# Kernel tuning notes

Measured on AMD Instinct MI355X. Metric: run time of the kernel, lower is better.

Reference implementation:

```python
import jax, jax.numpy as jnp
import numpy as np

BAND_LOW_MAX = 500.0
BAND_MID_MAX = 2000.0
ENERGY_THRESHOLD = 0.5

V, NH, NM = 1024, 16384, 16384


def setup_inputs() -> dict:
    key = jax.random.key(0)
    k1, k2, k3, k4, k5, k6 = jax.random.split(key, 6)
    harm_amps = jax.random.uniform(k1, (V, NH), dtype=jnp.float32)
    noise_mags = jax.random.uniform(k2, (V, NM), dtype=jnp.float32)
    # fundamental in [50, 1000) Hz so low/mid/high bands are all populated
    f0_hz = 50.0 + 950.0 * jax.random.uniform(k3, (V,), dtype=jnp.float32)
    competition_weight = 0.1 + jax.random.uniform(k4, (V,), dtype=jnp.float32)
    withdrawal = jax.random.uniform(k5, (V, 3), dtype=jnp.float32)  # [low, mid, high]
    is_active = jax.random.randint(k6, (V,), 0, 2).astype(bool)
    return {
        'harm_amps': harm_amps,
        'noise_mags': noise_mags,
        'f0_hz': f0_hz,
        'competition_weight': competition_weight,
        'withdrawal': withdrawal,
        'is_active': is_active,
    }


def reference(harm_amps, noise_mags, f0_hz, competition_weight, withdrawal, is_active):
    dt = harm_amps.dtype
    nh = harm_amps.shape[-1]
    actf = is_active.astype(dt)                     # [V]
    n_active = jnp.sum(is_active)

    harmonics = jnp.arange(1, nh + 1, dtype=dt)     # [NH]
    freqs = f0_hz[:, None] * harmonics[None, :]     # [V, NH]
    # bands partition the harmonics: 0=low (<500), 1=mid [500,2000), 2=high (>=2000)
    band_idx = (freqs >= BAND_LOW_MAX).astype(jnp.int32) + (freqs >= BAND_MID_MAX).astype(jnp.int32)  # [V, NH]

    # per-voice per-band energy (inactive voices contribute 0, as in the torch code)
    energy = jnp.stack(
        [jnp.sum(jnp.where(band_idx == b, harm_amps, jnp.zeros((), dt)), axis=-1) for b in range(3)],
        axis=1,
    ) * actf[:, None]                               # [V, 3]

    total_energy = jnp.sum(energy, axis=0)          # [3]
    total_weight = jnp.sum(competition_weight * actf)

    claim_ratio = competition_weight / jnp.maximum(total_weight, 1e-6)  # [V]
    my_share = claim_ratio * ENERGY_THRESHOLD                           # [V]
    excess = energy - my_share[:, None]                                 # [V, 3]
    excess_ratio = excess / jnp.maximum(energy, 1e-6)                   # [V, 3]
    reduction = jnp.maximum(0.3, 1.0 - withdrawal * excess_ratio * 0.5) # [V, 3]

    # reduction only applies when band is crowded, voice has energy, and voice exceeds its share
    apply = (total_energy[None, :] > ENERGY_THRESHOLD) & (energy > 0.0) & (excess > 0.0) & is_active[:, None]
    gain = jnp.where(apply, reduction, jnp.ones((), dt))                # [V, 3]

    elem_gain = jnp.take_along_axis(gain, band_idx, axis=1)             # [V, NH]
    harm_new = harm_amps * elem_gain

    total_before = jnp.sum(harm_amps, axis=-1)      # [V]
    total_after = jnp.sum(harm_new, axis=-1)        # [V]
    noise_scale = jnp.where(total_before > 1e-6, total_after / total_before, jnp.ones((), dt))
    noise_new = noise_mags * jnp.where(is_active, noise_scale, jnp.ones((), dt))[:, None]

    # inactive voices pass through unchanged
    harm_new = jnp.where(is_active[:, None], harm_new, harm_amps)

    # fewer than 2 active voices -> no competition at all
    changed = n_active >= 2
    harm_out = jnp.where(changed, harm_new, harm_amps)
    noise_out = jnp.where(changed, noise_new, noise_mags)
    # concat harm and noise outputs along last axis: [V, NH + NM]
    return jnp.concatenate([harm_out, noise_out], axis=-1)
```

## Files before the change

kernel.cpp:

```cpp
#include <hip/hip_runtime.h>

#define V   1024
#define NH  16384
#define NM  16384

#define BAND_LOW_MAX    500.0f
#define BAND_MID_MAX    2000.0f
#define ENERGY_THRESHOLD 0.5f

typedef float f32x4 __attribute__((ext_vector_type(4)));

__global__ __launch_bounds__(256)
void pass1_band_energy(const float* __restrict__ harm,
                       const float* __restrict__ f0_hz,
                       float* __restrict__ Eraw ) {
    const int v = blockIdx.x;
    const float f0 = f0_hz[v];
    const f32x4* h4 = (const f32x4*)(harm + (size_t)v * NH);

    float e0 = 0.f, e1 = 0.f, e2 = 0.f;
    for (int c = threadIdx.x; c < NH / 4; c += 256) {
        f32x4 a = h4[c];
        const int hbase = c * 4;
        #pragma unroll
        for (int j = 0; j < 4; ++j) {
            float amp  = a[j];
            float freq = f0 * (float)(hbase + j + 1);
            if (freq < BAND_LOW_MAX)       e0 += amp;
            else if (freq < BAND_MID_MAX)  e1 += amp;
            else                           e2 += amp;
        }
    }
    for (int off = 32; off > 0; off >>= 1) {
        e0 += __shfl_down(e0, off);
        e1 += __shfl_down(e1, off);
        e2 += __shfl_down(e2, off);
    }
    __shared__ float s[3][4];
    const int wid  = threadIdx.x >> 6;
    const int lane = threadIdx.x & 63;
    if (lane == 0) { s[0][wid] = e0; s[1][wid] = e1; s[2][wid] = e2; }
    __syncthreads();
    if (threadIdx.x == 0) {
        float t0 = 0.f, t1 = 0.f, t2 = 0.f;
        #pragma unroll
        for (int i = 0; i < 4; ++i) { t0 += s[0][i]; t1 += s[1][i]; t2 += s[2][i]; }
        Eraw[v * 3 + 0] = t0;
        Eraw[v * 3 + 1] = t1;
        Eraw[v * 3 + 2] = t2;
    }
}

__global__ __launch_bounds__(1024)
void pass2_gains(const float* __restrict__ Eraw,
                 const float* __restrict__ cw,
                 const float* __restrict__ wd,
                 const int*   __restrict__ is_active,
                 float* __restrict__ gains ) {
    const int v = threadIdx.x;
    const float e0 = Eraw[v * 3 + 0];
    const float e1 = Eraw[v * 3 + 1];
    const float e2 = Eraw[v * 3 + 2];
    const bool  act  = (is_active[v] != 0);
    const float actf = act ? 1.0f : 0.0f;
    const float w    = cw[v];

    const float ea0 = e0 * actf, ea1 = e1 * actf, ea2 = e2 * actf;

    float r0 = ea0, r1 = ea1, r2 = ea2, r3 = w * actf, r4 = actf;
    for (int off = 32; off > 0; off >>= 1) {
        r0 += __shfl_down(r0, off);
        r1 += __shfl_down(r1, off);
        r2 += __shfl_down(r2, off);
        r3 += __shfl_down(r3, off);
        r4 += __shfl_down(r4, off);
    }
    __shared__ float s[5][16];
    __shared__ float tot[5];
    const int wid  = threadIdx.x >> 6;
    const int lane = threadIdx.x & 63;
    if (lane == 0) {
        s[0][wid] = r0; s[1][wid] = r1; s[2][wid] = r2;
        s[3][wid] = r3; s[4][wid] = r4;
    }
    __syncthreads();
    if (threadIdx.x < 5) {
        float t = 0.f;
        #pragma unroll
        for (int i = 0; i < 16; ++i) t += s[threadIdx.x][i];
        tot[threadIdx.x] = t;
    }
    __syncthreads();

    const float TE[3] = { tot[0], tot[1], tot[2] };
    const float TW    = tot[3];
    const bool changed = (tot[4] >= 1.5f);

    const float claim = w / fmaxf(TW, 1e-6f);
    const float share = claim * ENERGY_THRESHOLD;

    const float ea[3] = { ea0, ea1, ea2 };
    const float er[3] = { e0, e1, e2 };

    const float tbefore = e0 + e1 + e2;
    float tafter = 0.f;
    float g[3];
    #pragma unroll
    for (int b = 0; b < 3; ++b) {
        const float excess = ea[b] - share;
        const float exr    = excess / fmaxf(ea[b], 1e-6f);
        const float red    = fmaxf(0.3f, 1.0f - wd[v * 3 + b] * exr * 0.5f);
        const bool apply   = (TE[b] > ENERGY_THRESHOLD) && (ea[b] > 0.0f) &&
                             (excess > 0.0f) && act;
        const float gb = apply ? red : 1.0f;
        tafter += gb * er[b];
        g[b] = changed ? gb : 1.0f;
    }

    const float nscale = (tbefore > 1e-6f) ? (tafter / tbefore) : 1.0f;
    const float nse = (changed && act) ? nscale : 1.0f;

    gains[v * 4 + 0] = g[0];
    gains[v * 4 + 1] = g[1];
    gains[v * 4 + 2] = g[2];
    gains[v * 4 + 3] = nse;
}

__global__ __launch_bounds__(256)
void pass3_apply(const float* __restrict__ harm,
                 const float* __restrict__ noise,
                 const float* __restrict__ f0_hz,
                 const float* __restrict__ gains,
                 float* __restrict__ out) {
    const int v   = blockIdx.x >> 4;
    const int seg = (blockIdx.x & 15) << 9;
    const int c0  = seg + threadIdx.x;

    f32x4* outrow = (f32x4*)out + (size_t)v * 8192;

    if (seg < 4096) {
        const float f0 = f0_hz[v];
        const float g0 = gains[v * 4 + 0];
        const float g1 = gains[v * 4 + 1];
        const float g2 = gains[v * 4 + 2];
        const f32x4* hrow = (const f32x4*)harm + (size_t)v * 4096;
        const f32x4 a0 = hrow[c0];
        const f32x4 a1 = hrow[c0 + 256];
        f32x4 o0, o1;
        #pragma unroll
        for (int j = 0; j < 4; ++j) {
            const float fr0 = f0 * (float)(c0 * 4 + j + 1);
            const float fr1 = f0 * (float)((c0 + 256) * 4 + j + 1);
            const float ga = (fr0 < BAND_LOW_MAX) ? g0 : (fr0 < BAND_MID_MAX) ? g1 : g2;
            const float gb = (fr1 < BAND_LOW_MAX) ? g0 : (fr1 < BAND_MID_MAX) ? g1 : g2;
            o0[j] = a0[j] * ga;
            o1[j] = a1[j] * gb;
        }
        __builtin_nontemporal_store(o0, outrow + c0);
        __builtin_nontemporal_store(o1, outrow + c0 + 256);
    } else {
        const float ns = gains[v * 4 + 3];
        const f32x4* nrow = (const f32x4*)noise + (size_t)v * 4096 - 4096;
        const f32x4 n0 = __builtin_nontemporal_load(nrow + c0);
        const f32x4 n1 = __builtin_nontemporal_load(nrow + c0 + 256);
        f32x4 o0, o1;
        o0 = n0 * ns;
        o1 = n1 * ns;
        __builtin_nontemporal_store(o0, outrow + c0);
        __builtin_nontemporal_store(o1, outrow + c0 + 256);
    }
}

extern "C" void kernel_launch(void* const* d_in, const int* in_sizes, int n_in,
                              void* d_out, int out_size, void* d_ws, size_t ws_size,
                              hipStream_t stream) {
    const float* harm  = (const float*)d_in[0];
    const float* noise = (const float*)d_in[1];
    const float* f0    = (const float*)d_in[2];
    const float* cw    = (const float*)d_in[3];
    const float* wd    = (const float*)d_in[4];
    const int*   act   = (const int*)d_in[5];
    float* out = (float*)d_out;

    float* Eraw  = (float*)d_ws;
    float* gains = Eraw + 4096;

    pass1_band_energy<<<V, 256, 0, stream>>>(harm, f0, Eraw);
    pass2_gains<<<1, 1024, 0, stream>>>(Eraw, cw, wd, act, gains);
    pass3_apply<<<V * 16, 256, 0, stream>>>(harm, noise, f0, gains, out);
}
```

Before: 60.22 us.

## Fuse three passes into one cooperative kernel with register-held harmonics

Replaces the three-kernel pipeline with a single cooperative kernel. Each block loads its voice's harmonic row into registers once, computes band energies, and publishes per-voice stats. After a grid-wide sync, every block redundantly reduces the totals, computes its own gains, and writes the harmonic and noise outputs. This removes the second read of harm and two launch boundaries, at the cost of 64 live vector registers per thread, a grid barrier, and the requirement that all 1024 blocks be co-resident; if the cooperative launch fails it falls back to the old three-kernel path.

After: 179.7 us. 198% more time.

```diff
diff --git a/kernel.cpp b/kernel.cpp
--- a/kernel.cpp
+++ b/kernel.cpp
@@ -1,4 +1,7 @@
 #include <hip/hip_runtime.h>
+#include <hip/hip_cooperative_groups.h>
+
+namespace cg = cooperative_groups;
 
 #define V   1024
 #define NH  16384
@@ -10,25 +13,153 @@
 
 typedef float f32x4 __attribute__((ext_vector_type(4)));
 
+__global__ __launch_bounds__(256, 4)
+void fused_all(const float* __restrict__ harm,
+               const float* __restrict__ noise,
+               const float* __restrict__ f0_hz,
+               const float* __restrict__ cw,
+               const float* __restrict__ wd,
+               const int*   __restrict__ is_active,
+               float* __restrict__ out,
+               float* stats ) {
+    const int v   = blockIdx.x;
+    const int tid = threadIdx.x;
+    const float f0 = f0_hz[v];
+
+    const f32x4* hrow = (const f32x4*)harm + (size_t)v * 4096;
+    f32x4 h[16];
+    #pragma unroll
+    for (int k = 0; k < 16; ++k)
+        h[k] = __builtin_nontemporal_load(hrow + tid + k * 256);
+
+    float e0 = 0.f, e1 = 0.f, e2 = 0.f;
+    #pragma unroll
+    for (int k = 0; k < 16; ++k) {
+        const int hbase = (tid + k * 256) * 4;
+        #pragma unroll
+        for (int j = 0; j < 4; ++j) {
+            const float freq = f0 * (float)(hbase + j + 1);
+            const float amp  = h[k][j];
+            if (freq < BAND_LOW_MAX)       e0 += amp;
+            else if (freq < BAND_MID_MAX)  e1 += amp;
+            else                           e2 += amp;
+        }
+    }
+    for (int off = 32; off > 0; off >>= 1) {
+        e0 += __shfl_down(e0, off);
+        e1 += __shfl_down(e1, off);
+        e2 += __shfl_down(e2, off);
+    }
+    __shared__ float s1[3][4];
+    __shared__ float ebc[3];
+    const int wid  = tid >> 6;
+    const int lane = tid & 63;
+    if (lane == 0) { s1[0][wid] = e0; s1[1][wid] = e1; s1[2][wid] = e2; }
+    __syncthreads();
+    if (tid == 0) {
+        const float t0 = s1[0][0] + s1[0][1] + s1[0][2] + s1[0][3];
+        const float t1 = s1[1][0] + s1[1][1] + s1[1][2] + s1[1][3];
+        const float t2 = s1[2][0] + s1[2][1] + s1[2][2] + s1[2][3];
+        ebc[0] = t0; ebc[1] = t1; ebc[2] = t2;
+        const float af = (is_active[v] != 0) ? 1.0f : 0.0f;
+        stats[0 * V + v] = t0 * af;
+        stats[1 * V + v] = t1 * af;
+        stats[2 * V + v] = t2 * af;
+        stats[3 * V + v] = cw[v] * af;
+        stats[4 * V + v] = af;
+    }
+
+    cg::this_grid().sync();
+
+    float r[5];
+    #pragma unroll
+    for (int p = 0; p < 5; ++p) {
+        const f32x4 x = ((const f32x4*)(stats + p * V))[tid];
+        r[p] = (x[0] + x[1]) + (x[2] + x[3]);
+    }
+    #pragma unroll
+    for (int p = 0; p < 5; ++p)
+        for (int off = 32; off > 0; off >>= 1)
+            r[p] += __shfl_down(r[p], off);
+    __shared__ float s2[5][4];
+    if (lane == 0) {
+        #pragma unroll
+        for (int p = 0; p < 5; ++p) s2[p][wid] = r[p];
+    }
+    __syncthreads();
+    const float TE0 = s2[0][0] + s2[0][1] + s2[0][2] + s2[0][3];
+    const float TE1 = s2[1][0] + s2[1][1] + s2[1][2] + s2[1][3];
+    const float TE2 = s2[2][0] + s2[2][1] + s2[2][2] + s2[2][3];
+    const float TW  = s2[3][0] + s2[3][1] + s2[3][2] + s2[3][3];
+    const float NA  = s2[4][0] + s2[4][1] + s2[4][2] + s2[4][3];
+
+    const bool  act  = (is_active[v] != 0);
+    const float af   = act ? 1.0f : 0.0f;
+    const bool  changed = (NA >= 1.5f);
+    const float w     = cw[v];
+    const float share = (w / fmaxf(TW, 1e-6f)) * ENERGY_THRESHOLD;
+
+    const float er[3] = { ebc[0], ebc[1], ebc[2] };
+    const float TE[3] = { TE0, TE1, TE2 };
+
+    const float tbefore = er[0] + er[1] + er[2];
+    float tafter = 0.f;
+    float g[3];
+    #pragma unroll
+    for (int b = 0; b < 3; ++b) {
+        const float ea     = er[b] * af;
+        const float excess = ea - share;
+        const float exr    = excess / fmaxf(ea, 1e-6f);
+        const float red    = fmaxf(0.3f, 1.0f - wd[v * 3 + b] * exr * 0.5f);
+        const bool apply   = (TE[b] > ENERGY_THRESHOLD) && (ea > 0.0f) &&
+                             (excess > 0.0f) && act;
+        const float gb = apply ? red : 1.0f;
+        tafter += gb * er[b];
+        g[b] = changed ? gb : 1.0f;
+    }
+    const float nscale = (tbefore > 1e-6f) ? (tafter / tbefore) : 1.0f;
+    const float nse    = (changed && act) ? nscale : 1.0f;
+    const float g0 = g[0], g1 = g[1], g2 = g[2];
+
+    f32x4* orow = (f32x4*)out + (size_t)v * 8192;
+    #pragma unroll
+    for (int k = 0; k < 16; ++k) {
+        const int hbase = (tid + k * 256) * 4;
+        f32x4 o;
+        #pragma unroll
+        for (int j = 0; j < 4; ++j) {
+            const float freq = f0 * (float)(hbase + j + 1);
+            const float gg = (freq < BAND_LOW_MAX) ? g0
+                           : (freq < BAND_MID_MAX) ? g1 : g2;
+            o[j] = h[k][j] * gg;
+        }
+        __builtin_nontemporal_store(o, orow + tid + k * 256);
+    }
+    const f32x4* nrow = (const f32x4*)noise + (size_t)v * 4096;
+    #pragma unroll
+    for (int k = 0; k < 16; ++k) {
+        const f32x4 n = __builtin_nontemporal_load(nrow + tid + k * 256);
+        __builtin_nontemporal_store(n * nse, orow + 4096 + tid + k * 256);
+    }
+}
+
 __global__ __launch_bounds__(256)
 void pass1_band_energy(const float* __restrict__ harm,
                        const float* __restrict__ f0_hz,
-                       float* __restrict__ Eraw ) {
+                       float* __restrict__ Eraw) {
     const int v = blockIdx.x;
     const float f0 = f0_hz[v];
     const f32x4* h4 = (const f32x4*)(harm + (size_t)v * NH);
-
     float e0 = 0.f, e1 = 0.f, e2 = 0.f;
     for (int c = threadIdx.x; c < NH / 4; c += 256) {
         f32x4 a = h4[c];
         const int hbase = c * 4;
         #pragma unroll
         for (int j = 0; j < 4; ++j) {
-            float amp  = a[j];
             float freq = f0 * (float)(hbase + j + 1);
-            if (freq < BAND_LOW_MAX)       e0 += amp;
-            else if (freq < BAND_MID_MAX)  e1 += amp;
-            else                           e2 += amp;
+            if (freq < BAND_LOW_MAX)       e0 += a[j];
+            else if (freq < BAND_MID_MAX)  e1 += a[j];
+            else                           e2 += a[j];
         }
     }
     for (int off = 32; off > 0; off >>= 1) {
@@ -37,17 +168,13 @@
         e2 += __shfl_down(e2, off);
     }
     __shared__ float s[3][4];
-    const int wid  = threadIdx.x >> 6;
-    const int lane = threadIdx.x & 63;
+    const int wid = threadIdx.x >> 6, lane = threadIdx.x & 63;
     if (lane == 0) { s[0][wid] = e0; s[1][wid] = e1; s[2][wid] = e2; }
     __syncthreads();
     if (threadIdx.x == 0) {
-        float t0 = 0.f, t1 = 0.f, t2 = 0.f;
-        #pragma unroll
-        for (int i = 0; i < 4; ++i) { t0 += s[0][i]; t1 += s[1][i]; t2 += s[2][i]; }
-        Eraw[v * 3 + 0] = t0;
-        Eraw[v * 3 + 1] = t1;
-        Eraw[v * 3 + 2] = t2;
+        Eraw[v * 3 + 0] = s[0][0] + s[0][1] + s[0][2] + s[0][3];
+        Eraw[v * 3 + 1] = s[1][0] + s[1][1] + s[1][2] + s[1][3];
+        Eraw[v * 3 + 2] = s[2][0] + s[2][1] + s[2][2] + s[2][3];
     }
 }
 
@@ -56,33 +183,23 @@
                  const float* __restrict__ cw,
                  const float* __restrict__ wd,
                  const int*   __restrict__ is_active,
-                 float* __restrict__ gains ) {
+                 float* __restrict__ gains) {
     const int v = threadIdx.x;
-    const float e0 = Eraw[v * 3 + 0];
-    const float e1 = Eraw[v * 3 + 1];
-    const float e2 = Eraw[v * 3 + 2];
-    const bool  act  = (is_active[v] != 0);
+    const float e0 = Eraw[v * 3 + 0], e1 = Eraw[v * 3 + 1], e2 = Eraw[v * 3 + 2];
+    const bool act = (is_active[v] != 0);
     const float actf = act ? 1.0f : 0.0f;
-    const float w    = cw[v];
-
+    const float w = cw[v];
     const float ea0 = e0 * actf, ea1 = e1 * actf, ea2 = e2 * actf;
-
     float r0 = ea0, r1 = ea1, r2 = ea2, r3 = w * actf, r4 = actf;
     for (int off = 32; off > 0; off >>= 1) {
-        r0 += __shfl_down(r0, off);
-        r1 += __shfl_down(r1, off);
-        r2 += __shfl_down(r2, off);
-        r3 += __shfl_down(r3, off);
+        r0 += __shfl_down(r0, off); r1 += __shfl_down(r1, off);
+        r2 += __shfl_down(r2, off); r3 += __shfl_down(r3, off);
         r4 += __shfl_down(r4, off);
     }
     __shared__ float s[5][16];
     __shared__ float tot[5];
-    const int wid  = threadIdx.x >> 6;
-    const int lane = threadIdx.x & 63;
-    if (lane == 0) {
-        s[0][wid] = r0; s[1][wid] = r1; s[2][wid] = r2;
-        s[3][wid] = r3; s[4][wid] = r4;
-    }
+    const int wid = threadIdx.x >> 6, lane = threadIdx.x & 63;
+    if (lane == 0) { s[0][wid]=r0; s[1][wid]=r1; s[2][wid]=r2; s[3][wid]=r3; s[4][wid]=r4; }
     __syncthreads();
     if (threadIdx.x < 5) {
         float t = 0.f;
@@ -91,39 +208,31 @@
         tot[threadIdx.x] = t;
     }
     __syncthreads();
-
     const float TE[3] = { tot[0], tot[1], tot[2] };
-    const float TW    = tot[3];
+    const float TW = tot[3];
     const bool changed = (tot[4] >= 1.5f);
-
-    const float claim = w / fmaxf(TW, 1e-6f);
-    const float share = claim * ENERGY_THRESHOLD;
-
+    const float share = (w / fmaxf(TW, 1e-6f)) * ENERGY_THRESHOLD;
     const float ea[3] = { ea0, ea1, ea2 };
     const float er[3] = { e0, e1, e2 };
-
     const float tbefore = e0 + e1 + e2;
     float tafter = 0.f;
     float g[3];
     #pragma unroll
     for (int b = 0; b < 3; ++b) {
         const float excess = ea[b] - share;
-        const float exr    = excess / fmaxf(ea[b], 1e-6f);
-        const float red    = fmaxf(0.3f, 1.0f - wd[v * 3 + b] * exr * 0.5f);
-        const bool apply   = (TE[b] > ENERGY_THRESHOLD) && (ea[b] > 0.0f) &&
-                             (excess > 0.0f) && act;
+        const float exr = excess / fmaxf(ea[b], 1e-6f);
+        const float red = fmaxf(0.3f, 1.0f - wd[v * 3 + b] * exr * 0.5f);
+        const bool apply = (TE[b] > ENERGY_THRESHOLD) && (ea[b] > 0.0f) &&
+                           (excess > 0.0f) && act;
         const float gb = apply ? red : 1.0f;
         tafter += gb * er[b];
         g[b] = changed ? gb : 1.0f;
     }
-
     const float nscale = (tbefore > 1e-6f) ? (tafter / tbefore) : 1.0f;
-    const float nse = (changed && act) ? nscale : 1.0f;
-
     gains[v * 4 + 0] = g[0];
     gains[v * 4 + 1] = g[1];
     gains[v * 4 + 2] = g[2];
-    gains[v * 4 + 3] = nse;
+    gains[v * 4 + 3] = (changed && act) ? nscale : 1.0f;
 }
 
 __global__ __launch_bounds__(256)
@@ -135,14 +244,10 @@
     const int v   = blockIdx.x >> 4;
     const int seg = (blockIdx.x & 15) << 9;
     const int c0  = seg + threadIdx.x;
-
     f32x4* outrow = (f32x4*)out + (size_t)v * 8192;
-
     if (seg < 4096) {
         const float f0 = f0_hz[v];
-        const float g0 = gains[v * 4 + 0];
-        const float g1 = gains[v * 4 + 1];
-        const float g2 = gains[v * 4 + 2];
+        const float g0 = gains[v*4+0], g1 = gains[v*4+1], g2 = gains[v*4+2];
         const f32x4* hrow = (const f32x4*)harm + (size_t)v * 4096;
         const f32x4 a0 = hrow[c0];
         const f32x4 a1 = hrow[c0 + 256];
@@ -151,10 +256,8 @@
         for (int j = 0; j < 4; ++j) {
             const float fr0 = f0 * (float)(c0 * 4 + j + 1);
             const float fr1 = f0 * (float)((c0 + 256) * 4 + j + 1);
-            const float ga = (fr0 < BAND_LOW_MAX) ? g0 : (fr0 < BAND_MID_MAX) ? g1 : g2;
-            const float gb = (fr1 < BAND_LOW_MAX) ? g0 : (fr1 < BAND_MID_MAX) ? g1 : g2;
-            o0[j] = a0[j] * ga;
-            o1[j] = a1[j] * gb;
+            o0[j] = a0[j] * ((fr0 < BAND_LOW_MAX) ? g0 : (fr0 < BAND_MID_MAX) ? g1 : g2);
+            o1[j] = a1[j] * ((fr1 < BAND_LOW_MAX) ? g0 : (fr1 < BAND_MID_MAX) ? g1 : g2);
         }
         __builtin_nontemporal_store(o0, outrow + c0);
         __builtin_nontemporal_store(o1, outrow + c0 + 256);
@@ -163,11 +266,8 @@
         const f32x4* nrow = (const f32x4*)noise + (size_t)v * 4096 - 4096;
         const f32x4 n0 = __builtin_nontemporal_load(nrow + c0);
         const f32x4 n1 = __builtin_nontemporal_load(nrow + c0 + 256);
-        f32x4 o0, o1;
-        o0 = n0 * ns;
-        o1 = n1 * ns;
-        __builtin_nontemporal_store(o0, outrow + c0);
-        __builtin_nontemporal_store(o1, outrow + c0 + 256);
+        __builtin_nontemporal_store(n0 * ns, outrow + c0);
+        __builtin_nontemporal_store(n1 * ns, outrow + c0 + 256);
     }
 }
 
@@ -180,12 +280,19 @@
     const float* cw    = (const float*)d_in[3];
     const float* wd    = (const float*)d_in[4];
     const int*   act   = (const int*)d_in[5];
-    float* out = (float*)d_out;
-
-    float* Eraw  = (float*)d_ws;
-    float* gains = Eraw + 4096;
-
-    pass1_band_energy<<<V, 256, 0, stream>>>(harm, f0, Eraw);
-    pass2_gains<<<1, 1024, 0, stream>>>(Eraw, cw, wd, act, gains);
-    pass3_apply<<<V * 16, 256, 0, stream>>>(harm, noise, f0, gains, out);
-}
+    float* out   = (float*)d_out;
+    float* stats = (float*)d_ws;
+
+    void* args[] = { (void*)&harm, (void*)&noise, (void*)&f0, (void*)&cw,
+                     (void*)&wd, (void*)&act, (void*)&out, (void*)&stats };
+    hipError_t err = hipLaunchCooperativeKernel((const void*)fused_all,
+                                                dim3(V), dim3(256),
+                                                args, 0, stream);
+    if (err != hipSuccess) {
+        float* Eraw  = (float*)d_ws;
+        float* gains = Eraw + 4096;
+        pass1_band_energy<<<V, 256, 0, stream>>>(harm, f0, Eraw);
+        pass2_gains<<<1, 1024, 0, stream>>>(Eraw, cw, wd, act, gains);
+        pass3_apply<<<V * 16, 256, 0, stream>>>(harm, noise, f0, gains, out);
+    }
+}
```
